# Kernel tuning notes

Measured on AMD Instinct MI355X. Metric: run time of the kernel, lower is better.

Reference implementation:

```python
import jax, jax.numpy as jnp
import numpy as np

DIL = 1  # dilation


def setup_inputs() -> dict:
    key = jax.random.key(0)
    k0, k1, k2, k3 = jax.random.split(key, 4)
    B, Cin, Cout, K, L, NR = 16, 256, 256, 3, 4096, 5
    x = jax.random.normal(k0, (B, Cin, L), jnp.float32)
    # kaiming-uniform-ish scale for conv kernels
    base_kernels = jax.random.normal(k1, (NR, Cout, Cin, K), jnp.float32) * (1.0 / np.sqrt(Cin * K))
    base_biases = jax.random.normal(k2, (NR, Cout), jnp.float32) * (1.0 / np.sqrt(Cin * K))
    # controller: Linear(Cin*K -> NR) followed by softmax over rules
    ctrl_w = jax.random.normal(k3, (Cin * K, NR), jnp.float32) * (1.0 / np.sqrt(Cin * K))
    ctrl_b = jnp.zeros((NR,), jnp.float32)
    return {"x": x, "base_kernels": base_kernels, "base_biases": base_biases,
            "ctrl_w": ctrl_w, "ctrl_b": ctrl_b}


def reference(x, base_kernels, base_biases, ctrl_w, ctrl_b):
    NR, Cout, Cin, K = base_kernels.shape
    B, _, L = x.shape
    pad = (K - 1) * DIL
    px = jnp.pad(x, ((0, 0), (0, 0), (pad, 0)))  # causal left pad -> (B, Cin, L+pad)

    # patches: padded_x.unfold(dim=2, size=K, step=1)[:, :, :L] -> (B, Cin, L, K)
    patches = jnp.stack([px[:, :, k:k + L] for k in range(K)], axis=-1)
    patches = patches.transpose(0, 2, 1, 3).reshape(B, L, Cin * K)  # (B, L, Cin*K)

    # controller -> normalized firing strengths (B, L, NR)
    fr = jax.nn.softmax(patches @ ctrl_w + ctrl_b, axis=-1)

    # all n_rules causal convs in one grouped-as-batched-output conv
    rhs = base_kernels.reshape(NR * Cout, Cin, K)
    conv = jax.lax.conv_general_dilated(
        px, rhs, window_strides=(1,), padding=[(0, 0)],
        rhs_dilation=(DIL,), dimension_numbers=("NCH", "OIH", "NCH"))  # (B, NR*Cout, L)
    conv = conv.reshape(B, NR, Cout, L) + base_biases[None, :, :, None]

    # weighted sum over experts: sum_n fr[b,l,n] * conv[b,n,o,l]
    return jnp.einsum("bnol,bln->bol", conv, fr)
```

## Files before the change

### kernel.cpp

```cpp
#include <hip/hip_runtime.h>
#include <hip/hip_bf16.h>

typedef __attribute__((ext_vector_type(4))) float floatx4;
typedef __attribute__((ext_vector_type(8))) short shortx8;

#define NB   16
#define CIN  256
#define COUT 256
#define KW   3
#define LL   4096
#define NR   5
#define QK   768
#define NP   65536

static __device__ __forceinline__ unsigned short bf16bits(float f) {
    __hip_bfloat16 h = __float2bfloat16(f);
    return __builtin_bit_cast(unsigned short, h);
}

static __device__ __forceinline__ void gload16(const void* g, void* l) {
    __builtin_amdgcn_global_load_lds(
        (const __attribute__((address_space(1))) void*)g,
        (__attribute__((address_space(3))) void*)l, 16, 0, 0);
}

__global__ void k_wprep(const float* __restrict__ bk, __hip_bfloat16* __restrict__ wb,
                        float* __restrict__ frz) {
    int i = blockIdx.x * 256 + threadIdx.x;
    if (i < NP * NR) frz[i] = 0.f;
    if (i >= NR * COUT * QK) return;
    int m = i / QK, q = i % QK;
    int o = (m / 80) * 16 + (m & 15);
    int r = (m % 80) / 16;
    int k = q >> 8, cin = q & 255;
    wb[i] = __float2bfloat16(bk[((r * COUT + o) * CIN + cin) * KW + k]);
}

__global__ void k_tfr(const float* __restrict__ x, const float* __restrict__ cw,
                      __hip_bfloat16* __restrict__ xt, float* __restrict__ logit) {
    __shared__ float t[66][65];
    __shared__ float cwsh[64 * 15];
    int l0 = blockIdx.x * 64, c0 = blockIdx.y * 64, b = blockIdx.z;
    int tid = threadIdx.x;
    int r16 = tid >> 4, q16 = tid & 15;

    for (int i = tid; i < 64 * 15; i += 256) cwsh[i] = cw[c0 * 15 + i];

    #pragma unroll
    for (int pass = 0; pass < 4; ++pass) {
        int cin = pass * 16 + r16;
        float4 v = *(const float4*)&x[((size_t)(b * CIN + c0 + cin)) * LL + l0 + q16 * 4];
        t[q16 * 4 + 2][cin] = v.x;
        t[q16 * 4 + 3][cin] = v.y;
        t[q16 * 4 + 4][cin] = v.z;
        t[q16 * 4 + 5][cin] = v.w;
    }
    if (tid < 128) {
        int cin = tid >> 1, j = tid & 1;
        float v = 0.f;
        if (l0 > 0) v = x[((size_t)(b * CIN + c0 + cin)) * LL + l0 - 2 + j];
        t[j][cin] = v;
    }
    __syncthreads();

    #pragma unroll
    for (int pass = 0; pass < 4; ++pass) {
        int lr = pass * 16 + r16;
        int c4 = q16 * 4;
        ushort4 u;
        u.x = bf16bits(t[lr + 2][c4 + 0]);
        u.y = bf16bits(t[lr + 2][c4 + 1]);
        u.z = bf16bits(t[lr + 2][c4 + 2]);
        u.w = bf16bits(t[lr + 2][c4 + 3]);
        *(ushort4*)&xt[((size_t)(b * LL + l0 + lr)) * CIN + c0 + c4] = u;
    }

    int p = tid >> 2, q = tid & 3;
    float lg[NR] = {0.f, 0.f, 0.f, 0.f, 0.f};
    #pragma unroll 4
    for (int ci = 0; ci < 16; ++ci) {
        int cin = q * 16 + ci;
        float x0 = t[p][cin], x1 = t[p + 1][cin], x2 = t[p + 2][cin];
        const float* w = &cwsh[cin * 15];
        #pragma unroll
        for (int n = 0; n < NR; ++n)
            lg[n] += x0 * w[n] + x1 * w[5 + n] + x2 * w[10 + n];
    }
    #pragma unroll
    for (int n = 0; n < NR; ++n) {
        lg[n] += __shfl_xor(lg[n], 1);
        lg[n] += __shfl_xor(lg[n], 2);
    }
    if (q == 0) {
        float* lp = &logit[(size_t)(b * LL + l0 + p) * NR];
        #pragma unroll
        for (int n = 0; n < NR; ++n) atomicAdd(&lp[n], lg[n]);
    }
}

__global__ void k_softmax(const float* __restrict__ cb, float* __restrict__ fr) {
    int p = blockIdx.x * 256 + threadIdx.x;
    if (p >= NP) return;
    float l2[NR];
    #pragma unroll
    for (int n = 0; n < NR; ++n) l2[n] = fr[(size_t)p * NR + n] + cb[n];
    float m = l2[0];
    #pragma unroll
    for (int n = 1; n < NR; ++n) m = fmaxf(m, l2[n]);
    float e[NR], s = 0.f;
    #pragma unroll
    for (int n = 0; n < NR; ++n) { e[n] = __expf(l2[n] - m); s += e[n]; }
    float inv = 1.f / s;
    #pragma unroll
    for (int n = 0; n < NR; ++n) fr[(size_t)p * NR + n] = e[n] * inv;
}

#define BUFSH 15936
#define WOFFS 8256
__global__ __launch_bounds__(256, 2)
void k_conv(const __hip_bfloat16* __restrict__ xt, const __hip_bfloat16* __restrict__ wb,
            const float* __restrict__ fr, const float* __restrict__ bias,
            float* __restrict__ out) {
    __shared__ __align__(16) short lds[2 * BUFSH];
    __shared__ float bs[80];

    int g = blockIdx.x;
    int pt = ((g >> 7) << 3) | (g & 7);
    int y  = (g >> 3) & 15;
    int p0 = pt * 256;
    int m0 = y * 80, o0 = y * 16;
    int b = p0 >> 12, l0 = p0 & (LL - 1);
    int tid = threadIdx.x;
    int lane = tid & 63, wn = tid >> 6;
    int quad = lane >> 4, l16 = lane & 15;

    const __hip_bfloat16* xb = xt + (size_t)b * (LL * CIN);

    if (tid < 80) bs[tid] = bias[(tid >> 4) * COUT + o0 + (tid & 15)];

    int xsrc[4];
    #pragma unroll
    for (int j = 0; j < 4; ++j) {
        int i = tid + j * 256;
        int rowp = i >> 2, cslot = i & 3;
        int cg = cslot ^ (((rowp + 2) >> 1) & 3);
        xsrc[j] = (l0 + rowp) * CIN + cg * 8;
    }
    int wsrc[4];
    #pragma unroll
    for (int j = 0; j < 4; ++j) {
        int i = tid + j * 256;
        int s = i >> 2, cslot = i & 3;
        int cg = cslot ^ ((s >> 1) & 3);
        int kh = s / 80, m = s - kh * 80;
        wsrc[j] = (i < 960) ? ((m0 + m) * QK + kh * 256 + cg * 8) : 0;
    }
    int hR = tid >> 2, hslot = tid & 3;
    int hcg = hslot;
    int hsrc = (l0 - 2 + hR) * CIN + hcg * 8;

    int boff[3][4], aoff[3][5];
    #pragma unroll
    for (int kh = 0; kh < 3; ++kh) {
        #pragma unroll
        for (int nf = 0; nf < 4; ++nf) {
            int row = wn * 64 + nf * 16 + l16 + kh;
            int phys = quad ^ ((row >> 1) & 3);
            boff[kh][nf] = row * 32 + phys * 8;
        }
        #pragma unroll
        for (int mf = 0; mf < NR; ++mf) {
            int s = kh * 80 + mf * 16 + l16;
            int phys = quad ^ ((s >> 1) & 3);
            aoff[kh][mf] = WOFFS + s * 32 + phys * 8;
        }
    }

    floatx4 acc[NR][4];
    #pragma unroll
    for (int mf = 0; mf < NR; ++mf)
        #pragma unroll
        for (int nf = 0; nf < 4; ++nf)
            acc[mf][nf] = (floatx4){0.f, 0.f, 0.f, 0.f};

    auto stage = [&](short* B, int ph) {
        const __hip_bfloat16* xp = xb + ph * 32;
        const __hip_bfloat16* wp = wb + ph * 32;
        uint4 hv = make_uint4(0u, 0u, 0u, 0u);
        if (l0 > 0 && tid < 8) hv = *(const uint4*)(xp + hsrc);
        #pragma unroll
        for (int j = 0; j < 4; ++j)
            gload16(xp + xsrc[j], B + 64 + (j * 256 + wn * 64) * 8);
        #pragma unroll
        for (int j = 0; j < 3; ++j)
            gload16(wp + wsrc[j], B + WOFFS + (j * 256 + wn * 64) * 8);
        if (wn < 3)
            gload16(wp + wsrc[3], B + WOFFS + (768 + wn * 64) * 8);
        if (tid < 8) *(uint4*)(B + tid * 8) = hv;
    };

    auto compute = [&](const short* B) {
        #pragma unroll
        for (int kh = 0; kh < 3; ++kh) {
            shortx8 bfrag[4], afrag[NR];
            #pragma unroll
            for (int nf = 0; nf < 4; ++nf)
                bfrag[nf] = *(const shortx8*)&B[boff[kh][nf]];
            #pragma unroll
            for (int mf = 0; mf < NR; ++mf)
                afrag[mf] = *(const shortx8*)&B[aoff[kh][mf]];
            #pragma unroll
            for (int mf = 0; mf < NR; ++mf)
                #pragma unroll
                for (int nf = 0; nf < 4; ++nf)
                    acc[mf][nf] = __builtin_amdgcn_mfma_f32_16x16x32_bf16(
                        afrag[mf], bfrag[nf], acc[mf][nf], 0, 0, 0);
        }
    };

    stage(&lds[0], 0);
    __syncthreads();
    for (int ph = 0; ph < 8; ph += 2) {
        stage(&lds[BUFSH], ph + 1);
        compute(&lds[0]);
        __syncthreads();
        if (ph < 6) stage(&lds[0], ph + 2);
        compute(&lds[BUFSH]);
        __syncthreads();
    }

    #pragma unroll
    for (int nf = 0; nf < 4; ++nf) {
        int colp = wn * 64 + nf * 16 + l16;
        const float* fp = fr + (size_t)(p0 + colp) * NR;
        float f0 = fp[0], f1 = fp[1], f2 = fp[2], f3 = fp[3], f4 = fp[4];
        #pragma unroll
        for (int j = 0; j < 4; ++j) {
            int olo = quad * 4 + j;
            float v = f0 * (acc[0][nf][j] + bs[0 * 16 + olo])
                    + f1 * (acc[1][nf][j] + bs[1 * 16 + olo])
                    + f2 * (acc[2][nf][j] + bs[2 * 16 + olo])
                    + f3 * (acc[3][nf][j] + bs[3 * 16 + olo])
                    + f4 * (acc[4][nf][j] + bs[4 * 16 + olo]);
            out[((size_t)(b * COUT + o0 + olo)) * LL + l0 + colp] = v;
        }
    }
}

extern "C" void kernel_launch(void* const* d_in, const int* in_sizes, int n_in,
                              void* d_out, int out_size, void* d_ws, size_t ws_size,
                              hipStream_t stream) {
    const float* x  = (const float*)d_in[0];
    const float* bk = (const float*)d_in[1];
    const float* bb = (const float*)d_in[2];
    const float* cw = (const float*)d_in[3];
    const float* cb = (const float*)d_in[4];
    float* out = (float*)d_out;

    char* ws = (char*)d_ws;
    __hip_bfloat16* xt = (__hip_bfloat16*)ws;
    __hip_bfloat16* wb = (__hip_bfloat16*)(ws + 33554432);
    float*          fr = (float*)(ws + 33554432 + 1966080);

    k_wprep<<<dim3((NR * COUT * QK + 255) / 256), dim3(256), 0, stream>>>(bk, wb, fr);
    k_tfr<<<dim3(LL / 64, CIN / 64, NB), dim3(256), 0, stream>>>(x, cw, xt, fr);
    k_softmax<<<dim3(NP / 256), dim3(256), 0, stream>>>(cb, fr);
    k_conv<<<dim3(NP / 256 * (COUT / 16)), dim3(256), 0, stream>>>(xt, wb, fr, bb, out);
}
```

Before: 264.4 us.

## Pad transposed input with zero rows and triple-buffer conv staging with fine waitcnt

The transposed bf16 input now has two zero-filled causal pad rows per batch, written by the weight-prep kernel. This lets the conv kernel fetch halo rows through async global-to-LDS loads instead of a register load guarded by a branch. The conv main loop moves from double to triple buffering: it issues two stages ahead, waits with explicit vmcnt counts and a single barrier per phase, and raises wave priority around the MFMA compute. LDS use grows to three 32KB buffers, which may limit occupancy at two blocks per CU.

```diff
diff --git a/kernel.cpp b/kernel.cpp
--- a/kernel.cpp
+++ b/kernel.cpp
@@ -9,6 +9,7 @@
 #define COUT 256
 #define KW   3
 #define LL   4096
+#define LLP  4098
 #define NR   5
 #define QK   768
 #define NP   65536
@@ -25,9 +26,13 @@
 }
 
 __global__ void k_wprep(const float* __restrict__ bk, __hip_bfloat16* __restrict__ wb,
-                        float* __restrict__ frz) {
+                        float* __restrict__ frz, __hip_bfloat16* __restrict__ xt) {
     int i = blockIdx.x * 256 + threadIdx.x;
     if (i < NP * NR) frz[i] = 0.f;
+    if (i < NB * 2 * CIN) {
+        int bb = i >> 9, rr = i & 511;
+        xt[(size_t)bb * LLP * CIN + rr] = __float2bfloat16(0.f);
+    }
     if (i >= NR * COUT * QK) return;
     int m = i / QK, q = i % QK;
     int o = (m / 80) * 16 + (m & 15);
@@ -72,7 +77,7 @@
         u.y = bf16bits(t[lr + 2][c4 + 1]);
         u.z = bf16bits(t[lr + 2][c4 + 2]);
         u.w = bf16bits(t[lr + 2][c4 + 3]);
-        *(ushort4*)&xt[((size_t)(b * LL + l0 + lr)) * CIN + c0 + c4] = u;
+        *(ushort4*)&xt[((size_t)(b * LLP + 2 + l0 + lr)) * CIN + c0 + c4] = u;
     }
 
     int p = tid >> 2, q = tid & 3;
@@ -115,13 +120,13 @@
     for (int n = 0; n < NR; ++n) fr[(size_t)p * NR + n] = e[n] * inv;
 }
 
-#define BUFSH 15936
-#define WOFFS 8256
+#define BUFSH 16384
+#define HWCH  1024
 __global__ __launch_bounds__(256, 2)
 void k_conv(const __hip_bfloat16* __restrict__ xt, const __hip_bfloat16* __restrict__ wb,
             const float* __restrict__ fr, const float* __restrict__ bias,
             float* __restrict__ out) {
-    __shared__ __align__(16) short lds[2 * BUFSH];
+    __shared__ __align__(16) short lds[3 * BUFSH];
     __shared__ float bs[80];
 
     int g = blockIdx.x;
@@ -134,45 +139,54 @@
     int lane = tid & 63, wn = tid >> 6;
     int quad = lane >> 4, l16 = lane & 15;
 
-    const __hip_bfloat16* xb = xt + (size_t)b * (LL * CIN);
+    const __hip_bfloat16* xb = xt + (size_t)b * (LLP * CIN);
 
     if (tid < 80) bs[tid] = bias[(tid >> 4) * COUT + o0 + (tid & 15)];
 
     int xsrc[4];
     #pragma unroll
     for (int j = 0; j < 4; ++j) {
-        int i = tid + j * 256;
-        int rowp = i >> 2, cslot = i & 3;
-        int cg = cslot ^ (((rowp + 2) >> 1) & 3);
-        xsrc[j] = (l0 + rowp) * CIN + cg * 8;
-    }
-    int wsrc[4];
+        int i = j * 256 + tid;
+        int row = i >> 2, cs = i & 3;
+        int cg = cs ^ ((row >> 1) & 3);
+        xsrc[j] = (2 + l0 + row) * CIN + cg * 8;
+    }
+    const __hip_bfloat16* hwp[4];
     #pragma unroll
     for (int j = 0; j < 4; ++j) {
-        int i = tid + j * 256;
-        int s = i >> 2, cslot = i & 3;
-        int cg = cslot ^ ((s >> 1) & 3);
-        int kh = s / 80, m = s - kh * 80;
-        wsrc[j] = (i < 960) ? ((m0 + m) * QK + kh * 256 + cg * 8) : 0;
-    }
-    int hR = tid >> 2, hslot = tid & 3;
-    int hcg = hslot;
-    int hsrc = (l0 - 2 + hR) * CIN + hcg * 8;
+        int c = j * 256 + tid;
+        if (c < 8) {
+            int h = c >> 2, cs = c & 3;
+            hwp[j] = xb + ((l0 + h) * CIN + cs * 8);
+        } else if (c < 968) {
+            int w = c - 8;
+            int s = w >> 2, cs = w & 3;
+            int cg = cs ^ ((s >> 1) & 3);
+            int kh = s / 80, m = s - kh * 80;
+            hwp[j] = wb + ((m0 + m) * QK + kh * 256 + cg * 8);
+        } else {
+            int w = c - 8;
+            int s = (w >> 2) - 240, cs = w & 3;
+            int cg = cs ^ ((s >> 1) & 3);
+            hwp[j] = wb + ((m0 + s) * QK + cg * 8);
+        }
+    }
 
     int boff[3][4], aoff[3][5];
     #pragma unroll
     for (int kh = 0; kh < 3; ++kh) {
         #pragma unroll
         for (int nf = 0; nf < 4; ++nf) {
-            int row = wn * 64 + nf * 16 + l16 + kh;
-            int phys = quad ^ ((row >> 1) & 3);
-            boff[kh][nf] = row * 32 + phys * 8;
+            int row = wn * 64 + nf * 16 + l16 + kh - 2;
+            if (row < 0)
+                boff[kh][nf] = (HWCH + (row + 2) * 4 + quad) * 8;
+            else
+                boff[kh][nf] = row * 32 + (quad ^ ((row >> 1) & 3)) * 8;
         }
         #pragma unroll
         for (int mf = 0; mf < NR; ++mf) {
             int s = kh * 80 + mf * 16 + l16;
-            int phys = quad ^ ((s >> 1) & 3);
-            aoff[kh][mf] = WOFFS + s * 32 + phys * 8;
+            aoff[kh][mf] = (HWCH + 8 + s * 4 + (quad ^ ((s >> 1) & 3))) * 8;
         }
     }
 
@@ -183,23 +197,19 @@
         for (int nf = 0; nf < 4; ++nf)
             acc[mf][nf] = (floatx4){0.f, 0.f, 0.f, 0.f};
 
-    auto stage = [&](short* B, int ph) {
+    auto stage = [&](int buf, int ph) {
+        short* B = &lds[buf * BUFSH];
         const __hip_bfloat16* xp = xb + ph * 32;
-        const __hip_bfloat16* wp = wb + ph * 32;
-        uint4 hv = make_uint4(0u, 0u, 0u, 0u);
-        if (l0 > 0 && tid < 8) hv = *(const uint4*)(xp + hsrc);
         #pragma unroll
         for (int j = 0; j < 4; ++j)
-            gload16(xp + xsrc[j], B + 64 + (j * 256 + wn * 64) * 8);
-        #pragma unroll
-        for (int j = 0; j < 3; ++j)
-            gload16(wp + wsrc[j], B + WOFFS + (j * 256 + wn * 64) * 8);
-        if (wn < 3)
-            gload16(wp + wsrc[3], B + WOFFS + (768 + wn * 64) * 8);
-        if (tid < 8) *(uint4*)(B + tid * 8) = hv;
+            gload16(xp + xsrc[j], B + (j * 256 + wn * 64) * 8);
+        #pragma unroll
+        for (int j = 0; j < 4; ++j)
+            gload16(hwp[j] + ph * 32, B + (HWCH + j * 256 + wn * 64) * 8);
     };
 
-    auto compute = [&](const short* B) {
+    auto compute = [&](int buf) {
+        const short* B = &lds[buf * BUFSH];
         #pragma unroll
         for (int kh = 0; kh < 3; ++kh) {
             shortx8 bfrag[4], afrag[NR];
@@ -218,15 +228,19 @@
         }
     };
 
-    stage(&lds[0], 0);
-    __syncthreads();
-    for (int ph = 0; ph < 8; ph += 2) {
-        stage(&lds[BUFSH], ph + 1);
-        compute(&lds[0]);
-        __syncthreads();
-        if (ph < 6) stage(&lds[0], ph + 2);
-        compute(&lds[BUFSH]);
-        __syncthreads();
+    stage(0, 0);
+    stage(1, 1);
+    #pragma unroll
+    for (int ph = 0; ph < 8; ++ph) {
+        if (ph == 0)      asm volatile("s_waitcnt vmcnt(8) lgkmcnt(0)" ::: "memory");
+        else if (ph < 7)  asm volatile("s_waitcnt vmcnt(8)" ::: "memory");
+        else              asm volatile("s_waitcnt vmcnt(0)" ::: "memory");
+        __builtin_amdgcn_s_barrier();
+        __builtin_amdgcn_sched_barrier(0);
+        if (ph < 6) stage((ph + 2) % 3, ph + 2);
+        __builtin_amdgcn_s_setprio(1);
+        compute(ph % 3);
+        __builtin_amdgcn_s_setprio(0);
     }
 
     #pragma unroll
@@ -259,10 +273,10 @@
 
     char* ws = (char*)d_ws;
     __hip_bfloat16* xt = (__hip_bfloat16*)ws;
-    __hip_bfloat16* wb = (__hip_bfloat16*)(ws + 33554432);
-    float*          fr = (float*)(ws + 33554432 + 1966080);
-
-    k_wprep<<<dim3((NR * COUT * QK + 255) / 256), dim3(256), 0, stream>>>(bk, wb, fr);
+    __hip_bfloat16* wb = (__hip_bfloat16*)(ws + 33570816);
+    float*          fr = (float*)(ws + 33570816 + 1966080);
+
+    k_wprep<<<dim3((NR * COUT * QK + 255) / 256), dim3(256), 0, stream>>>(bk, wb, fr, xt);
     k_tfr<<<dim3(LL / 64, CIN / 64, NB), dim3(256), 0, stream>>>(x, cw, xt, fr);
     k_softmax<<<dim3(NP / 256), dim3(256), 0, stream>>>(cb, fr);
     k_conv<<<dim3(NP / 256 * (COUT / 16)), dim3(256), 0, stream>>>(xt, wb, fr, bb, out);
```

New measurement: 310.1 us. 1.17x slower.

## Fuse softmax into transpose kernel, pad xt, read activations directly from global

Applied to the files above, without the earlier changes.

The transpose/logit kernel now loops over all 256 input channels per block, so it can compute the controller softmax in-register. This removes the atomicAdd logit accumulation, the zero-fill of the logit buffer and the separate softmax launch. The transposed activations get two zero rows of causal padding per batch, and the conv kernel loads its B fragments straight from global memory instead of staging them in LDS. Only the weights are now double-buffered in LDS, with a wider 64-channel stage and 8-way swizzle. The trade-off is more global-memory traffic and latency on the activation operand in the MFMA loop, plus fewer, longer tfr blocks.

```diff
diff --git a/kernel.cpp b/kernel.cpp
--- a/kernel.cpp
+++ b/kernel.cpp
@@ -9,6 +9,7 @@
 #define COUT 256
 #define KW   3
 #define LL   4096
+#define LLP  4098
 #define NR   5
 #define QK   768
 #define NP   65536
@@ -25,9 +26,12 @@
 }
 
 __global__ void k_wprep(const float* __restrict__ bk, __hip_bfloat16* __restrict__ wb,
-                        float* __restrict__ frz) {
+                        __hip_bfloat16* __restrict__ xt) {
     int i = blockIdx.x * 256 + threadIdx.x;
-    if (i < NP * NR) frz[i] = 0.f;
+    if (i < NB * 2 * CIN) {
+        int bb = i >> 9, rr = i & 511;
+        xt[(size_t)bb * LLP * CIN + rr] = __float2bfloat16(0.f);
+    }
     if (i >= NR * COUT * QK) return;
     int m = i / QK, q = i % QK;
     int o = (m / 80) * 16 + (m & 15);
@@ -37,54 +41,58 @@
 }
 
 __global__ void k_tfr(const float* __restrict__ x, const float* __restrict__ cw,
-                      __hip_bfloat16* __restrict__ xt, float* __restrict__ logit) {
+                      const float* __restrict__ cb,
+                      __hip_bfloat16* __restrict__ xt, float* __restrict__ fr) {
     __shared__ float t[66][65];
-    __shared__ float cwsh[64 * 15];
-    int l0 = blockIdx.x * 64, c0 = blockIdx.y * 64, b = blockIdx.z;
+    __shared__ float cwsh[QK * NR];
+    int l0 = blockIdx.x * 64, b = blockIdx.y;
     int tid = threadIdx.x;
     int r16 = tid >> 4, q16 = tid & 15;
-
-    for (int i = tid; i < 64 * 15; i += 256) cwsh[i] = cw[c0 * 15 + i];
-
-    #pragma unroll
-    for (int pass = 0; pass < 4; ++pass) {
-        int cin = pass * 16 + r16;
-        float4 v = *(const float4*)&x[((size_t)(b * CIN + c0 + cin)) * LL + l0 + q16 * 4];
-        t[q16 * 4 + 2][cin] = v.x;
-        t[q16 * 4 + 3][cin] = v.y;
-        t[q16 * 4 + 4][cin] = v.z;
-        t[q16 * 4 + 5][cin] = v.w;
-    }
-    if (tid < 128) {
-        int cin = tid >> 1, j = tid & 1;
-        float v = 0.f;
-        if (l0 > 0) v = x[((size_t)(b * CIN + c0 + cin)) * LL + l0 - 2 + j];
-        t[j][cin] = v;
-    }
-    __syncthreads();
-
-    #pragma unroll
-    for (int pass = 0; pass < 4; ++pass) {
-        int lr = pass * 16 + r16;
-        int c4 = q16 * 4;
-        ushort4 u;
-        u.x = bf16bits(t[lr + 2][c4 + 0]);
-        u.y = bf16bits(t[lr + 2][c4 + 1]);
-        u.z = bf16bits(t[lr + 2][c4 + 2]);
-        u.w = bf16bits(t[lr + 2][c4 + 3]);
-        *(ushort4*)&xt[((size_t)(b * LL + l0 + lr)) * CIN + c0 + c4] = u;
-    }
-
     int p = tid >> 2, q = tid & 3;
+
+    for (int i = tid; i < QK * NR; i += 256) cwsh[i] = cw[i];
+
     float lg[NR] = {0.f, 0.f, 0.f, 0.f, 0.f};
-    #pragma unroll 4
-    for (int ci = 0; ci < 16; ++ci) {
-        int cin = q * 16 + ci;
-        float x0 = t[p][cin], x1 = t[p + 1][cin], x2 = t[p + 2][cin];
-        const float* w = &cwsh[cin * 15];
-        #pragma unroll
-        for (int n = 0; n < NR; ++n)
-            lg[n] += x0 * w[n] + x1 * w[5 + n] + x2 * w[10 + n];
+    for (int ch = 0; ch < 4; ++ch) {
+        __syncthreads();
+        #pragma unroll
+        for (int pass = 0; pass < 4; ++pass) {
+            int cin = pass * 16 + r16;
+            float4 v = *(const float4*)&x[((size_t)(b * CIN + ch * 64 + cin)) * LL + l0 + q16 * 4];
+            t[q16 * 4 + 2][cin] = v.x;
+            t[q16 * 4 + 3][cin] = v.y;
+            t[q16 * 4 + 4][cin] = v.z;
+            t[q16 * 4 + 5][cin] = v.w;
+        }
+        if (tid < 128) {
+            int cin = tid >> 1, j = tid & 1;
+            float v = 0.f;
+            if (l0 > 0) v = x[((size_t)(b * CIN + ch * 64 + cin)) * LL + l0 - 2 + j];
+            t[j][cin] = v;
+        }
+        __syncthreads();
+
+        #pragma unroll
+        for (int pass = 0; pass < 4; ++pass) {
+            int lr = pass * 16 + r16;
+            int c4 = q16 * 4;
+            ushort4 u;
+            u.x = bf16bits(t[lr + 2][c4 + 0]);
+            u.y = bf16bits(t[lr + 2][c4 + 1]);
+            u.z = bf16bits(t[lr + 2][c4 + 2]);
+            u.w = bf16bits(t[lr + 2][c4 + 3]);
+            *(ushort4*)&xt[((size_t)(b * LLP + 2 + l0 + lr)) * CIN + ch * 64 + c4] = u;
+        }
+
+        #pragma unroll 4
+        for (int ci = 0; ci < 16; ++ci) {
+            int cin = q * 16 + ci;
+            float x0 = t[p][cin], x1 = t[p + 1][cin], x2 = t[p + 2][cin];
+            const float* w = &cwsh[(ch * 64 + cin) * 3 * NR];
+            #pragma unroll
+            for (int n = 0; n < NR; ++n)
+                lg[n] += x0 * w[n] + x1 * w[NR + n] + x2 * w[2 * NR + n];
+        }
     }
     #pragma unroll
     for (int n = 0; n < NR; ++n) {
@@ -92,36 +100,28 @@
         lg[n] += __shfl_xor(lg[n], 2);
     }
     if (q == 0) {
-        float* lp = &logit[(size_t)(b * LL + l0 + p) * NR];
-        #pragma unroll
-        for (int n = 0; n < NR; ++n) atomicAdd(&lp[n], lg[n]);
-    }
-}
-
-__global__ void k_softmax(const float* __restrict__ cb, float* __restrict__ fr) {
-    int p = blockIdx.x * 256 + threadIdx.x;
-    if (p >= NP) return;
-    float l2[NR];
-    #pragma unroll
-    for (int n = 0; n < NR; ++n) l2[n] = fr[(size_t)p * NR + n] + cb[n];
-    float m = l2[0];
-    #pragma unroll
-    for (int n = 1; n < NR; ++n) m = fmaxf(m, l2[n]);
-    float e[NR], s = 0.f;
-    #pragma unroll
-    for (int n = 0; n < NR; ++n) { e[n] = __expf(l2[n] - m); s += e[n]; }
-    float inv = 1.f / s;
-    #pragma unroll
-    for (int n = 0; n < NR; ++n) fr[(size_t)p * NR + n] = e[n] * inv;
-}
-
-#define BUFSH 15936
-#define WOFFS 8256
+        float l2[NR];
+        #pragma unroll
+        for (int n = 0; n < NR; ++n) l2[n] = lg[n] + cb[n];
+        float m = l2[0];
+        #pragma unroll
+        for (int n = 1; n < NR; ++n) m = fmaxf(m, l2[n]);
+        float e[NR], s = 0.f;
+        #pragma unroll
+        for (int n = 0; n < NR; ++n) { e[n] = __expf(l2[n] - m); s += e[n]; }
+        float inv = 1.f / s;
+        #pragma unroll
+        for (int n = 0; n < NR; ++n) fr[(size_t)(b * LL + l0 + p) * NR + n] = e[n] * inv;
+    }
+}
+
+#define WCH   1920
+#define WBUF  15360
 __global__ __launch_bounds__(256, 2)
 void k_conv(const __hip_bfloat16* __restrict__ xt, const __hip_bfloat16* __restrict__ wb,
             const float* __restrict__ fr, const float* __restrict__ bias,
             float* __restrict__ out) {
-    __shared__ __align__(16) short lds[2 * BUFSH];
+    __shared__ __align__(16) short Wl[2 * WBUF];
     __shared__ float bs[80];
 
     int g = blockIdx.x;
@@ -134,47 +134,29 @@
     int lane = tid & 63, wn = tid >> 6;
     int quad = lane >> 4, l16 = lane & 15;
 
-    const __hip_bfloat16* xb = xt + (size_t)b * (LL * CIN);
+    const __hip_bfloat16* xb = xt + (size_t)b * (LLP * CIN);
 
     if (tid < 80) bs[tid] = bias[(tid >> 4) * COUT + o0 + (tid & 15)];
 
-    int xsrc[4];
-    #pragma unroll
-    for (int j = 0; j < 4; ++j) {
-        int i = tid + j * 256;
-        int rowp = i >> 2, cslot = i & 3;
-        int cg = cslot ^ (((rowp + 2) >> 1) & 3);
-        xsrc[j] = (l0 + rowp) * CIN + cg * 8;
-    }
-    int wsrc[4];
-    #pragma unroll
-    for (int j = 0; j < 4; ++j) {
-        int i = tid + j * 256;
-        int s = i >> 2, cslot = i & 3;
-        int cg = cslot ^ ((s >> 1) & 3);
-        int kh = s / 80, m = s - kh * 80;
-        wsrc[j] = (i < 960) ? ((m0 + m) * QK + kh * 256 + cg * 8) : 0;
-    }
-    int hR = tid >> 2, hslot = tid & 3;
-    int hcg = hslot;
-    int hsrc = (l0 - 2 + hR) * CIN + hcg * 8;
-
-    int boff[3][4], aoff[3][5];
-    #pragma unroll
-    for (int kh = 0; kh < 3; ++kh) {
-        #pragma unroll
-        for (int nf = 0; nf < 4; ++nf) {
-            int row = wn * 64 + nf * 16 + l16 + kh;
-            int phys = quad ^ ((row >> 1) & 3);
-            boff[kh][nf] = row * 32 + phys * 8;
-        }
-        #pragma unroll
-        for (int mf = 0; mf < NR; ++mf) {
-            int s = kh * 80 + mf * 16 + l16;
-            int phys = quad ^ ((s >> 1) & 3);
-            aoff[kh][mf] = WOFFS + s * 32 + phys * 8;
-        }
-    }
+    int wsrc[8];
+    #pragma unroll
+    for (int j = 0; j < 8; ++j) {
+        int i = j * 256 + tid;
+        if (i < WCH) {
+            int s = i >> 3, cs = i & 7;
+            int cg = cs ^ (s & 7);
+            int kh = s / 80, m = s - kh * 80;
+            wsrc[j] = (m0 + m) * QK + kh * 256 + cg * 8;
+        } else wsrc[j] = 0;
+    }
+
+    const __hip_bfloat16* bbase[4];
+    #pragma unroll
+    for (int nf = 0; nf < 4; ++nf)
+        bbase[nf] = xb + (size_t)(l0 + wn * 64 + nf * 16 + l16) * CIN + quad * 8;
+
+    int abase0 = l16 * 64 + ((quad    ) ^ (l16 & 7)) * 8;
+    int abase1 = l16 * 64 + ((quad + 4) ^ (l16 & 7)) * 8;
 
     floatx4 acc[NR][4];
     #pragma unroll
@@ -183,49 +165,47 @@
         for (int nf = 0; nf < 4; ++nf)
             acc[mf][nf] = (floatx4){0.f, 0.f, 0.f, 0.f};
 
-    auto stage = [&](short* B, int ph) {
-        const __hip_bfloat16* xp = xb + ph * 32;
-        const __hip_bfloat16* wp = wb + ph * 32;
-        uint4 hv = make_uint4(0u, 0u, 0u, 0u);
-        if (l0 > 0 && tid < 8) hv = *(const uint4*)(xp + hsrc);
-        #pragma unroll
-        for (int j = 0; j < 4; ++j)
-            gload16(xp + xsrc[j], B + 64 + (j * 256 + wn * 64) * 8);
-        #pragma unroll
-        for (int j = 0; j < 3; ++j)
-            gload16(wp + wsrc[j], B + WOFFS + (j * 256 + wn * 64) * 8);
-        if (wn < 3)
-            gload16(wp + wsrc[3], B + WOFFS + (768 + wn * 64) * 8);
-        if (tid < 8) *(uint4*)(B + tid * 8) = hv;
+    auto stageW = [&](int buf, int ph) {
+        short* B = &Wl[buf * WBUF];
+        const __hip_bfloat16* wp = wb + ph * 64;
+        #pragma unroll
+        for (int j = 0; j < 8; ++j) {
+            int i = j * 256 + tid;
+            if (j < 7 || i < WCH)
+                gload16(wp + wsrc[j], B + i * 8);
+        }
     };
 
-    auto compute = [&](const short* B) {
+    auto compute = [&](int buf, int ph) {
+        const short* W = &Wl[buf * WBUF];
         #pragma unroll
         for (int kh = 0; kh < 3; ++kh) {
-            shortx8 bfrag[4], afrag[NR];
             #pragma unroll
-            for (int nf = 0; nf < 4; ++nf)
-                bfrag[nf] = *(const shortx8*)&B[boff[kh][nf]];
-            #pragma unroll
-            for (int mf = 0; mf < NR; ++mf)
-                afrag[mf] = *(const shortx8*)&B[aoff[kh][mf]];
-            #pragma unroll
-            for (int mf = 0; mf < NR; ++mf)
+            for (int csi = 0; csi < 2; ++csi) {
+                shortx8 bfrag[4], afrag[NR];
                 #pragma unroll
                 for (int nf = 0; nf < 4; ++nf)
-                    acc[mf][nf] = __builtin_amdgcn_mfma_f32_16x16x32_bf16(
-                        afrag[mf], bfrag[nf], acc[mf][nf], 0, 0, 0);
+                    bfrag[nf] = *(const shortx8*)(bbase[nf] + kh * CIN + ph * 64 + csi * 32);
+                int ab = csi ? abase1 : abase0;
+                #pragma unroll
+                for (int mf = 0; mf < NR; ++mf)
+                    afrag[mf] = *(const shortx8*)&W[(kh * 80 + mf * 16) * 64 + ab];
+                #pragma unroll
+                for (int mf = 0; mf < NR; ++mf)
+                    #pragma unroll
+                    for (int nf = 0; nf < 4; ++nf)
+                        acc[mf][nf] = __builtin_amdgcn_mfma_f32_16x16x32_bf16(
+                            afrag[mf], bfrag[nf], acc[mf][nf], 0, 0, 0);
+            }
         }
     };
 
-    stage(&lds[0], 0);
+    stageW(0, 0);
     __syncthreads();
-    for (int ph = 0; ph < 8; ph += 2) {
-        stage(&lds[BUFSH], ph + 1);
-        compute(&lds[0]);
-        __syncthreads();
-        if (ph < 6) stage(&lds[0], ph + 2);
-        compute(&lds[BUFSH]);
+    #pragma unroll
+    for (int ph = 0; ph < 4; ++ph) {
+        if (ph < 3) stageW((ph + 1) & 1, ph + 1);
+        compute(ph & 1, ph);
         __syncthreads();
     }
 
@@ -259,11 +239,10 @@
 
     char* ws = (char*)d_ws;
     __hip_bfloat16* xt = (__hip_bfloat16*)ws;
-    __hip_bfloat16* wb = (__hip_bfloat16*)(ws + 33554432);
-    float*          fr = (float*)(ws + 33554432 + 1966080);
-
-    k_wprep<<<dim3((NR * COUT * QK + 255) / 256), dim3(256), 0, stream>>>(bk, wb, fr);
-    k_tfr<<<dim3(LL / 64, CIN / 64, NB), dim3(256), 0, stream>>>(x, cw, xt, fr);
-    k_softmax<<<dim3(NP / 256), dim3(256), 0, stream>>>(cb, fr);
+    __hip_bfloat16* wb = (__hip_bfloat16*)(ws + 33570816);
+    float*          fr = (float*)(ws + 33570816 + 1966080);
+
+    k_wprep<<<dim3((NR * COUT * QK + 255) / 256), dim3(256), 0, stream>>>(bk, wb, xt);
+    k_tfr<<<dim3(LL / 64, NB), dim3(256), 0, stream>>>(x, cw, cb, xt, fr);
     k_conv<<<dim3(NP / 256 * (COUT / 16)), dim3(256), 0, stream>>>(xt, wb, fr, bb, out);
 }
```

Result: slower. 345.6 us (+30.7%).
